# Performance work log

Hardware: AMD Instinct MI355X
Metric: run time of the kernel (lower is better)

The kernel has to match this reference:

```python
import jax, jax.numpy as jnp
import numpy as np
import math

NUM_HEADS = 12
LN_EPS = 1e-5


def _band_mask(seq_len, level):
    # level 0 -> +/-2 window, level 1 -> +/-5 window, else full attention
    if level == 0:
        w = 2
    elif level == 1:
        w = 5
    else:
        return jnp.zeros((seq_len, seq_len), dtype=jnp.float32)
    i = jnp.arange(seq_len)
    inside = jnp.abs(i[:, None] - i[None, :]) <= w
    return jnp.where(inside, 0.0, -jnp.inf).astype(jnp.float32)


def setup_inputs() -> dict:
    key = jax.random.key(0)
    ks = jax.random.split(key, 8)
    B, S, H = 8, 1000, 768
    init = 0.02
    return {
        "features": jax.random.normal(ks[0], (B, S, H), jnp.float32),
        "pos_emb": jax.random.normal(ks[1], (1000, H), jnp.float32) * init,
        "Wq": jax.random.normal(ks[2], (H, H), jnp.float32) * init,
        "bq": jnp.zeros((H,), jnp.float32),
        "Wk": jax.random.normal(ks[3], (H, H), jnp.float32) * init,
        "bk": jnp.zeros((H,), jnp.float32),
        "Wv": jax.random.normal(ks[4], (H, H), jnp.float32) * init,
        "bv": jnp.zeros((H,), jnp.float32),
        "Wo": jax.random.normal(ks[5], (H, H), jnp.float32) * init,
        "bo": jnp.zeros((H,), jnp.float32),
        "ln_g": jnp.ones((H,), jnp.float32),
        "ln_b": jnp.zeros((H,), jnp.float32),
        "level": 0,
    }


def reference(features, pos_emb, Wq, bq, Wk, bk, Wv, bv, Wo, bo, ln_g, ln_b, level):
    B, S, H = features.shape
    nh = NUM_HEADS
    hd = H // nh
    # level-specific positional encoding (level_specific=True path)
    scale = 1.0 + 0.1 * level
    x = features + pos_emb[:S][None, :, :] * scale

    def proj(W, b):
        y = jnp.einsum('bsh,oh->bso', x, W) + b  # torch Linear: x @ W.T + b
        return y.reshape(B, S, nh, hd).transpose(0, 2, 1, 3)  # [B, nh, S, hd]

    Q = proj(Wq, bq)
    K = proj(Wk, bk)
    V = proj(Wv, bv)

    scores = jnp.einsum('bhqd,bhkd->bhqk', Q, K) / math.sqrt(hd)
    scores = scores + _band_mask(S, level)[None, None, :, :]
    attn = jax.nn.softmax(scores, axis=-1)  # dropout is identity (eval / p=0)
    ctx = jnp.einsum('bhqk,bhkd->bhqd', attn, V)
    ctx = ctx.transpose(0, 2, 1, 3).reshape(B, S, H)

    out = jnp.einsum('bsh,oh->bso', ctx, Wo) + bo
    y = out + features
    mu = jnp.mean(y, axis=-1, keepdims=True)
    var = jnp.var(y, axis=-1, keepdims=True)
    return (y - mu) / jnp.sqrt(var + LN_EPS) * ln_g + ln_b
```

## Files before the change

### kernel.cpp

```cpp
#include <hip/hip_runtime.h>
#include <hip/hip_bf16.h>
#include <cstddef>

typedef __attribute__((ext_vector_type(8))) short bf16x8;
typedef __attribute__((ext_vector_type(4))) float f32x4;

static __device__ __forceinline__ unsigned short f2bf(float f) {
    unsigned int u = __float_as_uint(f);
    u += 0x7fffu + ((u >> 16) & 1u);
    return (unsigned short)(u >> 16);
}
static __device__ __forceinline__ float bf2f(unsigned short h) {
    return __uint_as_float(((unsigned int)h) << 16);
}

#define B_ 8
#define S_ 1000
#define H_ 768
#define NH_ 12
#define HD_ 64
#define M_ 8000
#define HC_ 2304

__global__ __launch_bounds__(256)
void prep_all_kernel(const float* __restrict__ feat, const float* __restrict__ pos,
                     const int* __restrict__ level, unsigned short* __restrict__ xb,
                     const float* __restrict__ wq, const float* __restrict__ wk,
                     const float* __restrict__ wv, const float* __restrict__ wo,
                     unsigned short* __restrict__ wdst) {
    const size_t NX = (size_t)M_ * H_ / 4;
    const size_t WSZ = (size_t)H_ * H_;
    size_t gid = (size_t)blockIdx.x * blockDim.x + threadIdx.x;
    if (gid < NX) {
        size_t e = gid * 4;
        float sc = 1.0f + 0.1f * (float)level[0];
        const float4 f = *reinterpret_cast<const float4*>(&feat[e]);
        size_t pe = e % ((size_t)S_ * H_);
        const float4 p = *reinterpret_cast<const float4*>(&pos[pe]);
        ushort4 o;
        o.x = f2bf(f.x + sc * p.x);
        o.y = f2bf(f.y + sc * p.y);
        o.z = f2bf(f.z + sc * p.z);
        o.w = f2bf(f.w + sc * p.w);
        *reinterpret_cast<ushort4*>(&xb[e]) = o;
    } else {
        size_t e = (gid - NX) * 4;
        if (e >= 4 * WSZ) return;
        const float* src; size_t off;
        if (e < WSZ)          { src = wq; off = e; }
        else if (e < 2 * WSZ) { src = wk; off = e - WSZ; }
        else if (e < 3 * WSZ) { src = wv; off = e - 2 * WSZ; }
        else                  { src = wo; off = e - 3 * WSZ; }
        const float4 f = *reinterpret_cast<const float4*>(&src[off]);
        ushort4 o;
        o.x = f2bf(f.x); o.y = f2bf(f.y); o.z = f2bf(f.z); o.w = f2bf(f.w);
        *reinterpret_cast<ushort4*>(&wdst[e]) = o;
    }
}

__global__ __launch_bounds__(512, 4)
void gemm_qkv3(const unsigned short* __restrict__ A,
               const unsigned short* __restrict__ Bw,
               const float* __restrict__ b0, const float* __restrict__ b1,
               const float* __restrict__ b2,
               unsigned short* __restrict__ outB) {
    const int K = H_;
    __shared__ char lds[73728];
    const int tid = threadIdx.x, lane = tid & 63, wid = tid >> 6;
    const int wr = wid >> 2, wc = wid & 3;
    const int fr = lane & 15, fq = lane >> 4;

    const int nwg = gridDim.x;
    const int q = nwg >> 3, r = nwg & 7;
    const int xcd = blockIdx.x & 7, idx = blockIdx.x >> 3;
    const int swz = (xcd < r) ? (xcd * (q + 1) + idx) : (r * (q + 1) + (xcd - r) * q + idx);
    const int ntn = HC_ / 256;
    const int bm = (swz / ntn) * 128;
    const int bn = (swz % ntn) * 256;

    const int srow = lane >> 2;
    const int scol = ((lane & 3) ^ ((lane >> 3) & 3)) * 8;

    auto stage = [&](int buf, int k0) {
        char* base = lds + buf * 24576;
        int ar = bm + wid * 16 + srow;
        ar = ar < M_ ? ar : M_ - 1;
        __builtin_amdgcn_global_load_lds(
            (const __attribute__((address_space(1))) unsigned int*)(A + (size_t)ar * K + k0 + scol),
            (__attribute__((address_space(3))) unsigned int*)(base + wid * 1024), 16, 0, 0);
#pragma unroll
        for (int t = 0; t < 2; ++t) {
            const int c = wid * 2 + t;
            const int br = bn + c * 16 + srow;
            __builtin_amdgcn_global_load_lds(
                (const __attribute__((address_space(1))) unsigned int*)(Bw + (size_t)br * K + k0 + scol),
                (__attribute__((address_space(3))) unsigned int*)(base + 8192 + c * 1024), 16, 0, 0);
        }
    };

    f32x4 acc[4][4] = {};
    const int rsl = fq ^ ((fr >> 1) & 3);
    const int NT = K / 32;

    stage(0, 0);
    stage(1, 32);
    int bufsel = 0;
    for (int t = 0; t < NT; ++t) {
        if (t + 1 < NT) { asm volatile("s_waitcnt vmcnt(3)" ::: "memory"); }
        else            { asm volatile("s_waitcnt vmcnt(0)" ::: "memory"); }
        __builtin_amdgcn_s_barrier();
        if (t + 2 < NT) {
            int nb = bufsel + 2; nb = nb >= 3 ? nb - 3 : nb;
            stage(nb, (t + 2) * 32);
        }
        char* base = lds + bufsel * 24576;
        bufsel = bufsel + 1 == 3 ? 0 : bufsel + 1;

        bf16x8 af[4], bfv[4];
#pragma unroll
        for (int m = 0; m < 4; ++m) {
            const int row = wr * 64 + m * 16 + fr;
            af[m] = *reinterpret_cast<const bf16x8*>(base + row * 64 + rsl * 16);
        }
#pragma unroll
        for (int n = 0; n < 4; ++n) {
            const int row = wc * 64 + n * 16 + fr;
            bfv[n] = *reinterpret_cast<const bf16x8*>(base + 8192 + row * 64 + rsl * 16);
        }
        __builtin_amdgcn_s_setprio(1);
#pragma unroll
        for (int m = 0; m < 4; ++m)
#pragma unroll
            for (int n = 0; n < 4; ++n)
                acc[m][n] = __builtin_amdgcn_mfma_f32_16x16x32_bf16(bfv[n], af[m], acc[m][n], 0, 0, 0);
        __builtin_amdgcn_s_setprio(0);
    }

    const int colg = (bn < 768) ? bn : (bn < 1536) ? bn - 768 : bn - 1536;
    const float* bsel = (bn < 768) ? b0 : (bn < 1536) ? b1 : b2;
#pragma unroll
    for (int m = 0; m < 4; ++m) {
        const int row = bm + wr * 64 + m * 16 + fr;
        if (row >= M_) continue;
#pragma unroll
        for (int n = 0; n < 4; ++n) {
            const int cb = wc * 64 + n * 16 + fq * 4;
            const float4 bv = *reinterpret_cast<const float4*>(&bsel[colg + cb]);
            ushort4 o;
            o.x = f2bf(acc[m][n][0] + bv.x);
            o.y = f2bf(acc[m][n][1] + bv.y);
            o.z = f2bf(acc[m][n][2] + bv.z);
            o.w = f2bf(acc[m][n][3] + bv.w);
            *reinterpret_cast<ushort4*>(&outB[(size_t)row * HC_ + bn + cb]) = o;
        }
    }
}

__global__ __launch_bounds__(256, 3)
void gemm_out3(const unsigned short* __restrict__ A,
               const unsigned short* __restrict__ Bw,
               const float* __restrict__ b0,
               const float* __restrict__ resid,
               float* __restrict__ outF) {
    const int K = H_;
    __shared__ char lds[49152];
    const int tid = threadIdx.x, lane = tid & 63, wid = tid >> 6;
    const int wr = wid >> 1, wc = wid & 1;
    const int fr = lane & 15, fq = lane >> 4;

    const int nwg = gridDim.x;
    const int q = nwg >> 3, r = nwg & 7;
    const int xcd = blockIdx.x & 7, idx = blockIdx.x >> 3;
    const int swz = (xcd < r) ? (xcd * (q + 1) + idx) : (r * (q + 1) + (xcd - r) * q + idx);
    const int ntn = H_ / 128;
    const int bm = (swz / ntn) * 128;
    const int bn = (swz % ntn) * 128;

    const int srow = lane >> 2;
    const int scol = ((lane & 3) ^ ((lane >> 3) & 3)) * 8;

    auto stage = [&](int buf, int k0) {
        char* base = lds + buf * 16384;
#pragma unroll
        for (int t = 0; t < 2; ++t) {
            const int c = wid * 2 + t;
            int ar = bm + c * 16 + srow;
            ar = ar < M_ ? ar : M_ - 1;
            __builtin_amdgcn_global_load_lds(
                (const __attribute__((address_space(1))) unsigned int*)(A + (size_t)ar * K + k0 + scol),
                (__attribute__((address_space(3))) unsigned int*)(base + c * 1024), 16, 0, 0);
        }
#pragma unroll
        for (int t = 0; t < 2; ++t) {
            const int c = wid * 2 + t;
            const int br = bn + c * 16 + srow;
            __builtin_amdgcn_global_load_lds(
                (const __attribute__((address_space(1))) unsigned int*)(Bw + (size_t)br * K + k0 + scol),
                (__attribute__((address_space(3))) unsigned int*)(base + 8192 + c * 1024), 16, 0, 0);
        }
    };

    f32x4 acc[4][4] = {};
    const int rsl = fq ^ ((fr >> 1) & 3);
    const int NT = K / 32;

    stage(0, 0);
    stage(1, 32);
    int bufsel = 0;
    for (int t = 0; t < NT; ++t) {
        if (t + 1 < NT) { asm volatile("s_waitcnt vmcnt(4)" ::: "memory"); }
        else            { asm volatile("s_waitcnt vmcnt(0)" ::: "memory"); }
        __builtin_amdgcn_s_barrier();
        if (t + 2 < NT) {
            int nb = bufsel + 2; nb = nb >= 3 ? nb - 3 : nb;
            stage(nb, (t + 2) * 32);
        }
        char* base = lds + bufsel * 16384;
        bufsel = bufsel + 1 == 3 ? 0 : bufsel + 1;

        bf16x8 af[4], bfv[4];
#pragma unroll
        for (int m = 0; m < 4; ++m) {
            const int row = wr * 64 + m * 16 + fr;
            af[m] = *reinterpret_cast<const bf16x8*>(base + row * 64 + rsl * 16);
        }
#pragma unroll
        for (int n = 0; n < 4; ++n) {
            const int row = wc * 64 + n * 16 + fr;
            bfv[n] = *reinterpret_cast<const bf16x8*>(base + 8192 + row * 64 + rsl * 16);
        }
        __builtin_amdgcn_s_setprio(1);
#pragma unroll
        for (int m = 0; m < 4; ++m)
#pragma unroll
            for (int n = 0; n < 4; ++n)
                acc[m][n] = __builtin_amdgcn_mfma_f32_16x16x32_bf16(bfv[n], af[m], acc[m][n], 0, 0, 0);
        __builtin_amdgcn_s_setprio(0);
    }

#pragma unroll
    for (int m = 0; m < 4; ++m) {
        const int row = bm + wr * 64 + m * 16 + fr;
        if (row >= M_) continue;
#pragma unroll
        for (int n = 0; n < 4; ++n) {
            const int col = bn + wc * 64 + n * 16 + fq * 4;
            const float4 bv = *reinterpret_cast<const float4*>(&b0[col]);
            const float4 rv = *reinterpret_cast<const float4*>(&resid[(size_t)row * H_ + col]);
            float4 ov;
            ov.x = acc[m][n][0] + bv.x + rv.x;
            ov.y = acc[m][n][1] + bv.y + rv.y;
            ov.z = acc[m][n][2] + bv.z + rv.z;
            ov.w = acc[m][n][3] + bv.w + rv.w;
            *reinterpret_cast<float4*>(&outF[(size_t)row * H_ + col]) = ov;
        }
    }
}

__global__ __launch_bounds__(256)
void attn_kernel(const unsigned short* __restrict__ QKV,
                 unsigned short* __restrict__ ctx,
                 const int* __restrict__ level_p) {
    const int lane = threadIdx.x & 63;
    const int wv = threadIdx.x >> 6;
    const int qiw = lane >> 2;
    const int d0 = (lane & 3) * 16;

    const int qt = blockIdx.x & 15;
    const int h  = (blockIdx.x >> 4) % NH_;
    const int b  = blockIdx.x / (16 * NH_);
    const int i  = qt * 64 + wv * 16 + qiw;
    const bool valid = i < S_;
    const int iq = valid ? i : S_ - 1;

    const int lev = level_p[0];
    const int w = (lev == 0) ? 2 : (lev == 1) ? 5 : S_;

    const size_t qoff = (size_t)(b * S_ + iq) * HC_ + h * HD_ + d0;
    bf16x8 qa = *reinterpret_cast<const bf16x8*>(&QKV[qoff]);
    bf16x8 qb = *reinterpret_cast<const bf16x8*>(&QKV[qoff + 8]);
    float qf[16];
#pragma unroll
    for (int t = 0; t < 8; ++t) {
        qf[t]     = bf2f((unsigned short)qa[t]);
        qf[t + 8] = bf2f((unsigned short)qb[t]);
    }

    const int j0 = max(0, i - w), j1 = min(S_ - 1, i + w);
    float mx = -1e30f, l = 0.f;
    float acc[16];
#pragma unroll
    for (int t = 0; t < 16; ++t) acc[t] = 0.f;

    for (int jc = j0; jc <= j1; jc += 5) {
        float s[5];
        int jj[5];
#pragma unroll
        for (int t = 0; t < 5; ++t) {
            const int j = jc + t;
            jj[t] = j <= j1 ? j : j1;
            const size_t koff = (size_t)(b * S_ + jj[t]) * HC_ + 768 + h * HD_ + d0;
            bf16x8 ka = *reinterpret_cast<const bf16x8*>(&QKV[koff]);
            bf16x8 kb = *reinterpret_cast<const bf16x8*>(&QKV[koff + 8]);
            float p = 0.f;
#pragma unroll
            for (int d = 0; d < 8; ++d) {
                p = fmaf(qf[d], bf2f((unsigned short)ka[d]), p);
                p = fmaf(qf[d + 8], bf2f((unsigned short)kb[d]), p);
            }
            s[t] = p;
        }
#pragma unroll
        for (int t = 0; t < 5; ++t) s[t] += __shfl_xor(s[t], 1);
#pragma unroll
        for (int t = 0; t < 5; ++t) s[t] += __shfl_xor(s[t], 2);
#pragma unroll
        for (int t = 0; t < 5; ++t)
            s[t] = (jc + t <= j1) ? s[t] * 0.125f : -1e30f;

        float cm = fmaxf(fmaxf(fmaxf(s[0], s[1]), fmaxf(s[2], s[3])), s[4]);
        float nm = fmaxf(mx, cm);
        float corr = __expf(mx - nm);
        l *= corr;
#pragma unroll
        for (int t = 0; t < 16; ++t) acc[t] *= corr;
#pragma unroll
        for (int t = 0; t < 5; ++t) {
            const float e = __expf(s[t] - nm);
            l += e;
            const size_t voff = (size_t)(b * S_ + jj[t]) * HC_ + 1536 + h * HD_ + d0;
            bf16x8 va = *reinterpret_cast<const bf16x8*>(&QKV[voff]);
            bf16x8 vb = *reinterpret_cast<const bf16x8*>(&QKV[voff + 8]);
#pragma unroll
            for (int d = 0; d < 8; ++d) {
                acc[d]     = fmaf(e, bf2f((unsigned short)va[d]), acc[d]);
                acc[d + 8] = fmaf(e, bf2f((unsigned short)vb[d]), acc[d + 8]);
            }
        }
        mx = nm;
    }

    if (valid) {
        const float inv = 1.f / l;
        bf16x8 o0, o1;
#pragma unroll
        for (int t = 0; t < 8; ++t) {
            o0[t] = (short)f2bf(acc[t] * inv);
            o1[t] = (short)f2bf(acc[t + 8] * inv);
        }
        unsigned short* dst = &ctx[(size_t)(b * S_ + i) * H_ + h * HD_ + d0];
        *reinterpret_cast<bf16x8*>(dst) = o0;
        *reinterpret_cast<bf16x8*>(dst + 8) = o1;
    }
}

__global__ __launch_bounds__(256)
void ln_kernel(float* __restrict__ y, const float* __restrict__ g, const float* __restrict__ bta) {
    int row = blockIdx.x;
    int tid = threadIdx.x;
    float* p = y + (size_t)row * H_;
    float v[3];
    float s = 0.f, s2 = 0.f;
#pragma unroll
    for (int t = 0; t < 3; ++t) {
        v[t] = p[tid + t * 256];
        s += v[t];
        s2 += v[t] * v[t];
    }
#pragma unroll
    for (int o = 32; o; o >>= 1) {
        s  += __shfl_xor(s, o);
        s2 += __shfl_xor(s2, o);
    }
    __shared__ float ss[4], ss2[4];
    if ((tid & 63) == 0) { ss[tid >> 6] = s; ss2[tid >> 6] = s2; }
    __syncthreads();
    s  = ss[0] + ss[1] + ss[2] + ss[3];
    s2 = ss2[0] + ss2[1] + ss2[2] + ss2[3];
    float mu = s * (1.f / H_);
    float var = s2 * (1.f / H_) - mu * mu;
    float rs = rsqrtf(var + 1e-5f);
#pragma unroll
    for (int t = 0; t < 3; ++t) {
        int c = tid + t * 256;
        p[c] = (v[t] - mu) * rs * g[c] + bta[c];
    }
}

extern "C" void kernel_launch(void* const* d_in, const int* in_sizes, int n_in,
                              void* d_out, int out_size, void* d_ws, size_t ws_size,
                              hipStream_t stream) {
    const float* feat  = (const float*)d_in[0];
    const float* pos   = (const float*)d_in[1];
    const float* Wq    = (const float*)d_in[2];
    const float* bq    = (const float*)d_in[3];
    const float* Wk    = (const float*)d_in[4];
    const float* bk    = (const float*)d_in[5];
    const float* Wv    = (const float*)d_in[6];
    const float* bv    = (const float*)d_in[7];
    const float* Wo    = (const float*)d_in[8];
    const float* bo    = (const float*)d_in[9];
    const float* ln_g  = (const float*)d_in[10];
    const float* ln_b  = (const float*)d_in[11];
    const int*   level = (const int*)d_in[12];
    float* out = (float*)d_out;

    char* ws = (char*)d_ws;
    unsigned short* xb   = (unsigned short*)ws;
    unsigned short* Wcat = xb + (size_t)M_ * H_;
    unsigned short* QKVb = Wcat + (size_t)4 * H_ * H_;
    unsigned short* ctxb = QKVb + (size_t)M_ * HC_;

    const int nprep = (int)(((size_t)M_ * H_ / 4 + (size_t)4 * H_ * H_ / 4 + 255) / 256);
    prep_all_kernel<<<nprep, 256, 0, stream>>>(feat, pos, level, xb, Wq, Wk, Wv, Wo, Wcat);
    gemm_qkv3<<<63 * 9, 512, 0, stream>>>(xb, Wcat, bq, bk, bv, QKVb);
    attn_kernel<<<B_ * NH_ * 16, 256, 0, stream>>>(QKVb, ctxb, level);
    gemm_out3<<<63 * 6, 256, 0, stream>>>(ctxb, Wcat + (size_t)3 * H_ * H_, bo, feat, out);
    ln_kernel<<<M_, 256, 0, stream>>>(out, ln_g, ln_b);
}
```

Baseline: 113.9 us.

## Fuse output projection with LayerNorm and double-buffer QKV GEMM

Replaces the output-projection GEMM plus separate LayerNorm kernel with one kernel in which each 512-thread block computes full 768-wide rows for 32 tokens. It adds bias and residual, then reduces mean and variance in registers and LDS, which removes the fp32 round trip through global memory and one launch. The QKV GEMM moves from triple to double buffering with an extra barrier per step, cutting LDS so more blocks can be resident. In exchange the fused kernel runs only 250 blocks with a large B tile per block, which limits parallelism, and each block rereads the full Wo matrix.

```diff
diff --git a/kernel.cpp b/kernel.cpp
--- a/kernel.cpp
+++ b/kernel.cpp
@@ -58,14 +58,14 @@
     }
 }
 
-__global__ __launch_bounds__(512, 4)
-void gemm_qkv3(const unsigned short* __restrict__ A,
+__global__ __launch_bounds__(512, 6)
+void gemm_qkv4(const unsigned short* __restrict__ A,
                const unsigned short* __restrict__ Bw,
                const float* __restrict__ b0, const float* __restrict__ b1,
                const float* __restrict__ b2,
                unsigned short* __restrict__ outB) {
     const int K = H_;
-    __shared__ char lds[73728];
+    __shared__ char lds[49152];
     const int tid = threadIdx.x, lane = tid & 63, wid = tid >> 6;
     const int wr = wid >> 2, wc = wid & 3;
     const int fr = lane & 15, fq = lane >> 4;
@@ -103,19 +103,17 @@
     const int NT = K / 32;
 
     stage(0, 0);
-    stage(1, 32);
-    int bufsel = 0;
     for (int t = 0; t < NT; ++t) {
-        if (t + 1 < NT) { asm volatile("s_waitcnt vmcnt(3)" ::: "memory"); }
-        else            { asm volatile("s_waitcnt vmcnt(0)" ::: "memory"); }
+        const int cur = t & 1;
+        if (t + 1 < NT) {
+            stage(cur ^ 1, (t + 1) * 32);
+            asm volatile("s_waitcnt vmcnt(3)" ::: "memory");
+        } else {
+            asm volatile("s_waitcnt vmcnt(0)" ::: "memory");
+        }
         __builtin_amdgcn_s_barrier();
-        if (t + 2 < NT) {
-            int nb = bufsel + 2; nb = nb >= 3 ? nb - 3 : nb;
-            stage(nb, (t + 2) * 32);
-        }
-        char* base = lds + bufsel * 24576;
-        bufsel = bufsel + 1 == 3 ? 0 : bufsel + 1;
-
+
+        char* base = lds + cur * 24576;
         bf16x8 af[4], bfv[4];
 #pragma unroll
         for (int m = 0; m < 4; ++m) {
@@ -134,6 +132,7 @@
             for (int n = 0; n < 4; ++n)
                 acc[m][n] = __builtin_amdgcn_mfma_f32_16x16x32_bf16(bfv[n], af[m], acc[m][n], 0, 0, 0);
         __builtin_amdgcn_s_setprio(0);
+        __builtin_amdgcn_s_barrier();
     }
 
     const int colg = (bn < 768) ? bn : (bn < 1536) ? bn - 768 : bn - 1536;
@@ -156,102 +155,132 @@
     }
 }
 
-__global__ __launch_bounds__(256, 3)
-void gemm_out3(const unsigned short* __restrict__ A,
-               const unsigned short* __restrict__ Bw,
-               const float* __restrict__ b0,
-               const float* __restrict__ resid,
-               float* __restrict__ outF) {
+__global__ __launch_bounds__(512)
+void gemm_out_ln(const unsigned short* __restrict__ A,
+                 const unsigned short* __restrict__ Bw,
+                 const float* __restrict__ bo,
+                 const float* __restrict__ resid,
+                 const float* __restrict__ g, const float* __restrict__ lnb,
+                 float* __restrict__ outF) {
     const int K = H_;
-    __shared__ char lds[49152];
+    __shared__ char lds[102400];
+    __shared__ float sred[8][2][16][2];
     const int tid = threadIdx.x, lane = tid & 63, wid = tid >> 6;
-    const int wr = wid >> 1, wc = wid & 1;
     const int fr = lane & 15, fq = lane >> 4;
-
-    const int nwg = gridDim.x;
-    const int q = nwg >> 3, r = nwg & 7;
-    const int xcd = blockIdx.x & 7, idx = blockIdx.x >> 3;
-    const int swz = (xcd < r) ? (xcd * (q + 1) + idx) : (r * (q + 1) + (xcd - r) * q + idx);
-    const int ntn = H_ / 128;
-    const int bm = (swz / ntn) * 128;
-    const int bn = (swz % ntn) * 128;
+    const int bm = blockIdx.x * 32;
 
     const int srow = lane >> 2;
     const int scol = ((lane & 3) ^ ((lane >> 3) & 3)) * 8;
 
     auto stage = [&](int buf, int k0) {
-        char* base = lds + buf * 16384;
-#pragma unroll
-        for (int t = 0; t < 2; ++t) {
-            const int c = wid * 2 + t;
-            int ar = bm + c * 16 + srow;
-            ar = ar < M_ ? ar : M_ - 1;
+        char* base = lds + buf * 51200;
+        if (wid < 2) {
+            const int ar = bm + wid * 16 + srow;
             __builtin_amdgcn_global_load_lds(
                 (const __attribute__((address_space(1))) unsigned int*)(A + (size_t)ar * K + k0 + scol),
-                (__attribute__((address_space(3))) unsigned int*)(base + c * 1024), 16, 0, 0);
-        }
-#pragma unroll
-        for (int t = 0; t < 2; ++t) {
-            const int c = wid * 2 + t;
-            const int br = bn + c * 16 + srow;
+                (__attribute__((address_space(3))) unsigned int*)(base + wid * 1024), 16, 0, 0);
+        }
+#pragma unroll
+        for (int t = 0; t < 6; ++t) {
+            const int c = wid * 6 + t;
+            const int br = c * 16 + srow;
             __builtin_amdgcn_global_load_lds(
                 (const __attribute__((address_space(1))) unsigned int*)(Bw + (size_t)br * K + k0 + scol),
-                (__attribute__((address_space(3))) unsigned int*)(base + 8192 + c * 1024), 16, 0, 0);
+                (__attribute__((address_space(3))) unsigned int*)(base + 2048 + c * 1024), 16, 0, 0);
         }
     };
 
-    f32x4 acc[4][4] = {};
+    f32x4 acc[2][6] = {};
     const int rsl = fq ^ ((fr >> 1) & 3);
     const int NT = K / 32;
 
     stage(0, 0);
-    stage(1, 32);
-    int bufsel = 0;
     for (int t = 0; t < NT; ++t) {
-        if (t + 1 < NT) { asm volatile("s_waitcnt vmcnt(4)" ::: "memory"); }
-        else            { asm volatile("s_waitcnt vmcnt(0)" ::: "memory"); }
+        const int cur = t & 1;
+        if (t + 1 < NT) {
+            stage(cur ^ 1, (t + 1) * 32);
+            if (wid < 2) { asm volatile("s_waitcnt vmcnt(7)" ::: "memory"); }
+            else         { asm volatile("s_waitcnt vmcnt(6)" ::: "memory"); }
+        } else {
+            asm volatile("s_waitcnt vmcnt(0)" ::: "memory");
+        }
         __builtin_amdgcn_s_barrier();
-        if (t + 2 < NT) {
-            int nb = bufsel + 2; nb = nb >= 3 ? nb - 3 : nb;
-            stage(nb, (t + 2) * 32);
-        }
-        char* base = lds + bufsel * 16384;
-        bufsel = bufsel + 1 == 3 ? 0 : bufsel + 1;
-
-        bf16x8 af[4], bfv[4];
-#pragma unroll
-        for (int m = 0; m < 4; ++m) {
-            const int row = wr * 64 + m * 16 + fr;
+
+        char* base = lds + cur * 51200;
+        bf16x8 af[2], bfv[6];
+#pragma unroll
+        for (int m = 0; m < 2; ++m) {
+            const int row = m * 16 + fr;
             af[m] = *reinterpret_cast<const bf16x8*>(base + row * 64 + rsl * 16);
         }
 #pragma unroll
-        for (int n = 0; n < 4; ++n) {
-            const int row = wc * 64 + n * 16 + fr;
-            bfv[n] = *reinterpret_cast<const bf16x8*>(base + 8192 + row * 64 + rsl * 16);
+        for (int n = 0; n < 6; ++n) {
+            const int row = wid * 96 + n * 16 + fr;
+            bfv[n] = *reinterpret_cast<const bf16x8*>(base + 2048 + row * 64 + rsl * 16);
         }
         __builtin_amdgcn_s_setprio(1);
 #pragma unroll
-        for (int m = 0; m < 4; ++m)
-#pragma unroll
-            for (int n = 0; n < 4; ++n)
+        for (int m = 0; m < 2; ++m)
+#pragma unroll
+            for (int n = 0; n < 6; ++n)
                 acc[m][n] = __builtin_amdgcn_mfma_f32_16x16x32_bf16(bfv[n], af[m], acc[m][n], 0, 0, 0);
         __builtin_amdgcn_s_setprio(0);
-    }
-
-#pragma unroll
-    for (int m = 0; m < 4; ++m) {
-        const int row = bm + wr * 64 + m * 16 + fr;
-        if (row >= M_) continue;
-#pragma unroll
-        for (int n = 0; n < 4; ++n) {
-            const int col = bn + wc * 64 + n * 16 + fq * 4;
-            const float4 bv = *reinterpret_cast<const float4*>(&b0[col]);
+        __builtin_amdgcn_s_barrier();
+    }
+
+    float s[2] = {0.f, 0.f}, sq[2] = {0.f, 0.f};
+#pragma unroll
+    for (int m = 0; m < 2; ++m) {
+        const int row = bm + m * 16 + fr;
+#pragma unroll
+        for (int n = 0; n < 6; ++n) {
+            const int col = wid * 96 + n * 16 + fq * 4;
+            const float4 bv = *reinterpret_cast<const float4*>(&bo[col]);
             const float4 rv = *reinterpret_cast<const float4*>(&resid[(size_t)row * H_ + col]);
+            acc[m][n][0] += bv.x + rv.x;
+            acc[m][n][1] += bv.y + rv.y;
+            acc[m][n][2] += bv.z + rv.z;
+            acc[m][n][3] += bv.w + rv.w;
+#pragma unroll
+            for (int j = 0; j < 4; ++j) {
+                s[m]  += acc[m][n][j];
+                sq[m] += acc[m][n][j] * acc[m][n][j];
+            }
+        }
+    }
+#pragma unroll
+    for (int m = 0; m < 2; ++m) {
+        s[m]  += __shfl_xor(s[m], 16);  s[m]  += __shfl_xor(s[m], 32);
+        sq[m] += __shfl_xor(sq[m], 16); sq[m] += __shfl_xor(sq[m], 32);
+    }
+    if (fq == 0) {
+#pragma unroll
+        for (int m = 0; m < 2; ++m) { sred[wid][m][fr][0] = s[m]; sred[wid][m][fr][1] = sq[m]; }
+    }
+    __syncthreads();
+    float mu[2], rs[2];
+#pragma unroll
+    for (int m = 0; m < 2; ++m) {
+        float S = 0.f, Q = 0.f;
+#pragma unroll
+        for (int w = 0; w < 8; ++w) { S += sred[w][m][fr][0]; Q += sred[w][m][fr][1]; }
+        mu[m] = S * (1.f / H_);
+        float var = Q * (1.f / H_) - mu[m] * mu[m];
+        rs[m] = rsqrtf(var + 1e-5f);
+    }
+#pragma unroll
+    for (int m = 0; m < 2; ++m) {
+        const int row = bm + m * 16 + fr;
+#pragma unroll
+        for (int n = 0; n < 6; ++n) {
+            const int col = wid * 96 + n * 16 + fq * 4;
+            const float4 gv = *reinterpret_cast<const float4*>(&g[col]);
+            const float4 bb = *reinterpret_cast<const float4*>(&lnb[col]);
             float4 ov;
-            ov.x = acc[m][n][0] + bv.x + rv.x;
-            ov.y = acc[m][n][1] + bv.y + rv.y;
-            ov.z = acc[m][n][2] + bv.z + rv.z;
-            ov.w = acc[m][n][3] + bv.w + rv.w;
+            ov.x = (acc[m][n][0] - mu[m]) * rs[m] * gv.x + bb.x;
+            ov.y = (acc[m][n][1] - mu[m]) * rs[m] * gv.y + bb.y;
+            ov.z = (acc[m][n][2] - mu[m]) * rs[m] * gv.z + bb.z;
+            ov.w = (acc[m][n][3] - mu[m]) * rs[m] * gv.w + bb.w;
             *reinterpret_cast<float4*>(&outF[(size_t)row * H_ + col]) = ov;
         }
     }
@@ -351,39 +380,6 @@
         unsigned short* dst = &ctx[(size_t)(b * S_ + i) * H_ + h * HD_ + d0];
         *reinterpret_cast<bf16x8*>(dst) = o0;
         *reinterpret_cast<bf16x8*>(dst + 8) = o1;
-    }
-}
-
-__global__ __launch_bounds__(256)
-void ln_kernel(float* __restrict__ y, const float* __restrict__ g, const float* __restrict__ bta) {
-    int row = blockIdx.x;
-    int tid = threadIdx.x;
-    float* p = y + (size_t)row * H_;
-    float v[3];
-    float s = 0.f, s2 = 0.f;
-#pragma unroll
-    for (int t = 0; t < 3; ++t) {
-        v[t] = p[tid + t * 256];
-        s += v[t];
-        s2 += v[t] * v[t];
-    }
-#pragma unroll
-    for (int o = 32; o; o >>= 1) {
-        s  += __shfl_xor(s, o);
-        s2 += __shfl_xor(s2, o);
-    }
-    __shared__ float ss[4], ss2[4];
-    if ((tid & 63) == 0) { ss[tid >> 6] = s; ss2[tid >> 6] = s2; }
-    __syncthreads();
-    s  = ss[0] + ss[1] + ss[2] + ss[3];
-    s2 = ss2[0] + ss2[1] + ss2[2] + ss2[3];
-    float mu = s * (1.f / H_);
-    float var = s2 * (1.f / H_) - mu * mu;
-    float rs = rsqrtf(var + 1e-5f);
-#pragma unroll
-    for (int t = 0; t < 3; ++t) {
-        int c = tid + t * 256;
-        p[c] = (v[t] - mu) * rs * g[c] + bta[c];
     }
 }
 
@@ -413,8 +409,8 @@
 
     const int nprep = (int)(((size_t)M_ * H_ / 4 + (size_t)4 * H_ * H_ / 4 + 255) / 256);
     prep_all_kernel<<<nprep, 256, 0, stream>>>(feat, pos, level, xb, Wq, Wk, Wv, Wo, Wcat);
-    gemm_qkv3<<<63 * 9, 512, 0, stream>>>(xb, Wcat, bq, bk, bv, QKVb);
+    gemm_qkv4<<<63 * 9, 512, 0, stream>>>(xb, Wcat, bq, bk, bv, QKVb);
     attn_kernel<<<B_ * NH_ * 16, 256, 0, stream>>>(QKVb, ctxb, level);
-    gemm_out3<<<63 * 6, 256, 0, stream>>>(ctxb, Wcat + (size_t)3 * H_ * H_, bo, feat, out);
-    ln_kernel<<<M_, 256, 0, stream>>>(out, ln_g, ln_b);
-}
+    gemm_out_ln<<<250, 512, 0, stream>>>(ctxb, Wcat + (size_t)3 * H_ * H_, bo, feat,
+                                         ln_g, ln_b, out);
+}
```

New measurement: 343.3 us. 201% more time.
